# Optimization experiments

Measured on AMD Instinct MI355X. Metric: run time of the kernel, lower is better.

Reference implementation:

```python
import jax, jax.numpy as jnp
import numpy as np

N_HEADS, D_MODEL, D_K, D_V = 16, 1024, 64, 64
B, S = 2, 2048

def setup_inputs() -> dict:
    key = jax.random.key(0)
    k = jax.random.split(key, 7)
    s = 1.0 / np.sqrt(D_MODEL)
    return {
        "input_Q": jax.random.normal(k[0], (B, S, D_MODEL), jnp.float32),
        "input_K": jax.random.normal(k[1], (B, S, D_MODEL), jnp.float32),
        "input_V": jax.random.normal(k[2], (B, S, D_MODEL), jnp.float32),
        "W_Q": jax.random.normal(k[3], (D_MODEL, N_HEADS * D_K), jnp.float32) * s,
        "W_K": jax.random.normal(k[4], (D_MODEL, N_HEADS * D_K), jnp.float32) * s,
        "W_V": jax.random.normal(k[5], (D_MODEL, N_HEADS * D_V), jnp.float32) * s,
        "W_O": jax.random.normal(k[6], (N_HEADS * D_V, D_MODEL), jnp.float32) * s,
    }

def reference(input_Q, input_K, input_V, W_Q, W_K, W_V, W_O):
    b = input_Q.shape[0]
    # project and split heads: [b, h, s, d]
    Q = (input_Q @ W_Q).reshape(b, -1, N_HEADS, D_K).transpose(0, 2, 1, 3)
    K = (input_K @ W_K).reshape(b, -1, N_HEADS, D_K).transpose(0, 2, 1, 3)
    V = (input_V @ W_V).reshape(b, -1, N_HEADS, D_V).transpose(0, 2, 1, 3)
    scores = jnp.einsum("bhqd,bhkd->bhqk", Q, K) / np.sqrt(D_K)
    attn = jax.nn.softmax(scores, axis=-1)
    context = jnp.einsum("bhqk,bhkd->bhqd", attn, V)
    context = context.transpose(0, 2, 1, 3).reshape(b, -1, N_HEADS * D_V)
    out = context @ W_O + input_Q  # residual
    # LayerNorm instantiated fresh in torch forward -> gamma=1, beta=0
    mu = jnp.mean(out, axis=-1, keepdims=True)
    var = jnp.var(out, axis=-1, keepdims=True)
    return (out - mu) / jnp.sqrt(var + 1e-5)
```

## Files before the change

kernel.cpp:

```cpp
#include <hip/hip_runtime.h>
#include <hip/hip_bf16.h>
#include <cstdint>
#include <cstddef>

#define DEVFN __device__ __forceinline__

typedef __attribute__((ext_vector_type(8))) short short8;
typedef __attribute__((ext_vector_type(4))) float f32x4;
typedef __attribute__((ext_vector_type(16))) float f32x16;
typedef __attribute__((ext_vector_type(4))) unsigned short us4;

static constexpr int S_LEN = 2048;
static constexpr int DM    = 1024;
static constexpr int H     = 16;
static constexpr int DK    = 64;
static constexpr int BATCH = 2;
static constexpr int MROWS = BATCH * S_LEN;

DEVFN unsigned short f2bf(float f) {
  union { float f; unsigned int u; } x; x.f = f;
  unsigned int r = x.u + 0x7fffu + ((x.u >> 16) & 1u);
  return (unsigned short)(r >> 16);
}

DEVFN float fast_exp2(float x) { return __builtin_amdgcn_exp2f(x); }

DEVFN f32x4 mfma16(short8 a, short8 b, f32x4 c) {
  return __builtin_amdgcn_mfma_f32_16x16x32_bf16(a, b, c, 0, 0, 0);
}

DEVFN f32x16 mfma32(short8 a, short8 b, f32x16 c) {
  return __builtin_amdgcn_mfma_f32_32x32x16_bf16(a, b, c, 0, 0, 0);
}

DEVFN unsigned int cvtpk(float lo, float hi) {
  unsigned int r;
  asm("v_cvt_pk_bf16_f32 %0, %1, %2" : "=v"(r) : "v"(lo), "v"(hi));
  return r;
}

DEVFN void gload_lds16(const void* g, void* l) {
  __builtin_amdgcn_global_load_lds(
      (const __attribute__((address_space(1))) void*)g,
      (__attribute__((address_space(3))) void*)l, 16, 0, 0);
}

__global__ __launch_bounds__(256) void wt_transpose(
    const float* __restrict__ Wq, const float* __restrict__ Wk,
    const float* __restrict__ Wv, const float* __restrict__ Wo,
    unsigned short* __restrict__ Tq, unsigned short* __restrict__ Tk,
    unsigned short* __restrict__ Tv, unsigned short* __restrict__ To)
{
  const float* W = blockIdx.z == 0 ? Wq : blockIdx.z == 1 ? Wk : blockIdx.z == 2 ? Wv : Wo;
  unsigned short* T = blockIdx.z == 0 ? Tq : blockIdx.z == 1 ? Tk : blockIdx.z == 2 ? Tv : To;
  __shared__ float tile[32][33];
  int n0 = blockIdx.x * 32, k0 = blockIdx.y * 32;
  int tx = threadIdx.x & 31, ty = threadIdx.x >> 5;
#pragma unroll
  for (int i = 0; i < 4; ++i)
    tile[ty + 8 * i][tx] = W[(size_t)(k0 + ty + 8 * i) * DM + n0 + tx];
  __syncthreads();
#pragma unroll
  for (int i = 0; i < 4; ++i) {
    int n = ty + 8 * i;
    T[(size_t)(n0 + n) * DM + k0 + tx] = f2bf(tile[tx][n]);
  }
}

__global__ __launch_bounds__(256) void xcvt3(
    const float* __restrict__ X0, const float* __restrict__ X1,
    const float* __restrict__ X2, unsigned short* __restrict__ Y)
{
  const float* X = blockIdx.y == 0 ? X0 : blockIdx.y == 1 ? X1 : X2;
  unsigned short* Yz = Y + (size_t)blockIdx.y * MROWS * DM;
  const size_t i = ((size_t)blockIdx.x * 256 + threadIdx.x) * 8;
  float4 v0 = *(const float4*)(X + i);
  float4 v1 = *(const float4*)(X + i + 4);
  union { us4 u[2]; short8 s; } r;
  r.u[0].x = f2bf(v0.x); r.u[0].y = f2bf(v0.y); r.u[0].z = f2bf(v0.z); r.u[0].w = f2bf(v0.w);
  r.u[1].x = f2bf(v1.x); r.u[1].y = f2bf(v1.y); r.u[1].z = f2bf(v1.z); r.u[1].w = f2bf(v1.w);
  *(short8*)(Yz + i) = r.s;
}

__global__ __launch_bounds__(256, 3) void gemm_qkv(
    const unsigned short* __restrict__ Xb,
    const unsigned short* __restrict__ Tq, const unsigned short* __restrict__ Tk,
    const unsigned short* __restrict__ Tv,
    unsigned short* __restrict__ Qb, unsigned short* __restrict__ Kb,
    unsigned short* __restrict__ Vt)
{
  __shared__ __align__(16) unsigned short As[2][128 * 32];
  __shared__ __align__(16) unsigned short Bs[2][128 * 32];

  const int z = blockIdx.z;
  const unsigned short* A = Xb + (size_t)z * MROWS * DM;
  const unsigned short* T = z == 0 ? Tq : z == 1 ? Tk : Tv;

  const int tid = threadIdx.x;
  const int lane = tid & 63, w = tid >> 6;
  const int wm = w >> 1, wn = w & 1;
  const int lr = lane & 15, lg = lane >> 4;
  const int m0 = blockIdx.x * 128, n0 = blockIdx.y * 128;

  const int srw = lane >> 2, sch = lane & 3;

  auto stage = [&](int buf, int k0) {
#pragma unroll
    for (int i = 0; i < 2; ++i) {
      const int rr = (w * 2 + i) * 16 + srw;
      const int sc = (sch ^ ((rr >> 1) & 3)) * 8;
      gload_lds16(A + (size_t)(m0 + rr) * DM + k0 + sc, &As[buf][(w * 2 + i) * 512]);
      gload_lds16(T + (size_t)(n0 + rr) * DM + k0 + sc, &Bs[buf][(w * 2 + i) * 512]);
    }
  };

  f32x4 acc[4][4];
#pragma unroll
  for (int m = 0; m < 4; ++m)
#pragma unroll
    for (int n = 0; n < 4; ++n) acc[m][n] = (f32x4){0.f, 0.f, 0.f, 0.f};

  stage(0, 0);

  int buf = 0;
  for (int kt = 0; kt < DM / 32; ++kt) {
    if (kt + 1 < DM / 32) {
      stage(buf ^ 1, (kt + 1) * 32);
      asm volatile("s_waitcnt vmcnt(4)");
    } else {
      asm volatile("s_waitcnt vmcnt(0)");
    }
    __builtin_amdgcn_s_barrier();

    short8 af[4], bfr[4];
#pragma unroll
    for (int m = 0; m < 4; ++m) {
      const int row = wm * 64 + m * 16 + lr;
      const int ch = lg ^ ((row >> 1) & 3);
      af[m] = *(const short8*)&As[buf][row * 32 + ch * 8];
    }
#pragma unroll
    for (int n = 0; n < 4; ++n) {
      const int row = wn * 64 + n * 16 + lr;
      const int ch = lg ^ ((row >> 1) & 3);
      bfr[n] = *(const short8*)&Bs[buf][row * 32 + ch * 8];
    }
#pragma unroll
    for (int m = 0; m < 4; ++m)
#pragma unroll
      for (int n = 0; n < 4; ++n) acc[m][n] = mfma16(af[m], bfr[n], acc[m][n]);

    __builtin_amdgcn_s_barrier();
    buf ^= 1;
  }

  if (z < 2) {
    const float scale = (z == 0) ? 0.125f * 1.44269504088896f : 1.0f;
    unsigned short* out = z == 0 ? Qb : Kb;
#pragma unroll
    for (int m = 0; m < 4; ++m)
#pragma unroll
      for (int n = 0; n < 4; ++n) {
        int col = n0 + wn * 64 + n * 16 + lr;
        int h = col >> 6, d = col & 63;
#pragma unroll
        for (int r = 0; r < 4; ++r) {
          int row = m0 + wm * 64 + m * 16 + lg * 4 + r;
          int b = row >> 11, s = row & (S_LEN - 1);
          out[((size_t)(b * H + h) * S_LEN + s) * DK + d] = f2bf(acc[m][n][r] * scale);
        }
      }
  } else {
#pragma unroll
    for (int m = 0; m < 4; ++m)
#pragma unroll
      for (int n = 0; n < 4; ++n) {
        int col = n0 + wn * 64 + n * 16 + lr;
        int h = col >> 6, d = col & 63;
        int row = m0 + wm * 64 + m * 16 + lg * 4;
        int b = row >> 11, s = row & (S_LEN - 1);
        us4 u;
#pragma unroll
        for (int r = 0; r < 4; ++r) u[r] = f2bf(acc[m][n][r]);
        *(us4*)(Vt + ((size_t)(b * H + h) * DK + d) * S_LEN + s) = u;
      }
  }
}

__global__ __launch_bounds__(256, 2) void attn(
    const unsigned short* __restrict__ Qg, const unsigned short* __restrict__ Kg,
    const unsigned short* __restrict__ Vg, unsigned short* __restrict__ ctx)
{
  constexpr int KBLK = 64;
  constexpr int NT = S_LEN / KBLK;
  __shared__ __align__(16) unsigned short Ks[4][KBLK][DK];
  __shared__ __align__(16) unsigned short Vs[4][DK][KBLK];

  const int tid = threadIdx.x, lane = tid & 63, w = tid >> 6;
  const int l31 = lane & 31, hi = lane >> 5;

  const int orig = blockIdx.x;
  const int id = (orig & 7) * 64 + (orig >> 3);
  const int bh = id >> 4, qb = id & 15;
  const int b = bh >> 4, h = bh & 15;
  const int q = qb * 128 + w * 32 + l31;

  const unsigned short* Qbh = Qg + (size_t)bh * S_LEN * DK;
  const unsigned short* Kbh = Kg + (size_t)bh * S_LEN * DK;
  const unsigned short* Vbh = Vg + (size_t)bh * DK * S_LEN;

  const int srow = lane >> 3;
  const int sslot = ((lane & 7) ^ srow) * 8;

  auto stage = [&](int buf, int t) {
    const int kbase = t * KBLK;
#pragma unroll
    for (int c = 0; c < 2; ++c) {
      const int rbase = w * 8 + c * 32;
      gload_lds16(Kbh + (size_t)(kbase + rbase + srow) * DK + sslot, &Ks[buf][rbase][0]);
      gload_lds16(Vbh + (size_t)(rbase + srow) * S_LEN + kbase + sslot, &Vs[buf][rbase][0]);
    }
  };

  short8 qf[4];
#pragma unroll
  for (int kk = 0; kk < 4; ++kk)
    qf[kk] = *(const short8*)(Qbh + (size_t)q * DK + kk * 16 + hi * 8);

  f32x16 o0, o1;
#pragma unroll
  for (int i = 0; i < 16; ++i) { o0[i] = 0.f; o1[i] = 0.f; }
  float lrun = 0.f;

  const int swz = (l31 & 7) << 4;

  auto tile = [&](int buf) {
    const char* Kb = (const char*)&Ks[buf][0][0];
    const char* Vb = (const char*)&Vs[buf][0][0];

    f32x16 s0, s1;
#pragma unroll
    for (int i = 0; i < 16; ++i) { s0[i] = 0.f; s1[i] = 0.f; }
    __builtin_amdgcn_s_setprio(1);
#pragma unroll
    for (int kk = 0; kk < 4; ++kk) {
      const int cb = (kk * 32 + hi * 16) ^ swz;
      short8 ka0 = *(const short8*)(Kb + l31 * 128 + cb);
      short8 ka1 = *(const short8*)(Kb + (32 + l31) * 128 + cb);
      s0 = mfma32(ka0, qf[kk], s0);
      s1 = mfma32(ka1, qf[kk], s1);
    }
    __builtin_amdgcn_s_setprio(0);

#pragma unroll
    for (int i = 0; i < 16; ++i) {
      s0[i] = fast_exp2(s0[i]);
      s1[i] = fast_exp2(s1[i]);
    }

    float d0[16];
#pragma unroll
    for (int i = 0; i < 16; ++i) d0[i] = s0[i] + s1[i];
#pragma unroll
    for (int st = 8; st >= 1; st >>= 1)
#pragma unroll
      for (int i = 0; i < st; ++i) d0[i] = d0[i] + d0[i + st];
    lrun += d0[0] + __shfl_xor(d0[0], 32, 64);

    short8 pf[4];
#pragma unroll
    for (int sl = 0; sl < 4; ++sl) {
      const f32x16& sv = (sl & 2) ? s1 : s0;
      const int base = (sl & 1) * 8;
      const unsigned int a01 = cvtpk(sv[base + 0], sv[base + 1]);
      const unsigned int a23 = cvtpk(sv[base + 2], sv[base + 3]);
      const unsigned int b01 = cvtpk(sv[base + 4], sv[base + 5]);
      const unsigned int b23 = cvtpk(sv[base + 6], sv[base + 7]);
      const unsigned int x0 = __shfl_xor(hi ? a01 : b01, 32, 64);
      const unsigned int x1 = __shfl_xor(hi ? a23 : b23, 32, 64);
      union { unsigned int u[4]; short8 v; } pu;
      pu.u[0] = hi ? x0 : a01;
      pu.u[1] = hi ? x1 : a23;
      pu.u[2] = hi ? b01 : x0;
      pu.u[3] = hi ? b23 : x1;
      pf[sl] = pu.v;
    }

    __builtin_amdgcn_s_setprio(1);
#pragma unroll
    for (int sl = 0; sl < 4; ++sl) {
      const int cb = (sl * 32 + hi * 16) ^ swz;
      short8 va0 = *(const short8*)(Vb + l31 * 128 + cb);
      short8 va1 = *(const short8*)(Vb + (32 + l31) * 128 + cb);
      o0 = mfma32(va0, pf[sl], o0);
      o1 = mfma32(va1, pf[sl], o1);
    }
    __builtin_amdgcn_s_setprio(0);
  };

  stage(0, 0);
  stage(1, 1);

  for (int t = 0; t < NT; t += 2) {
    const bool more = (t + 2) < NT;
    if (more) {
      stage((t + 2) & 3, t + 2);
      stage((t + 3) & 3, t + 3);
      asm volatile("s_waitcnt vmcnt(8)");
    } else {
      asm volatile("s_waitcnt vmcnt(0)");
    }
    __builtin_amdgcn_s_barrier();
    tile(t & 3);
    tile((t + 1) & 3);
    __builtin_amdgcn_s_barrier();
  }

  const float rinv = 1.0f / lrun;
  unsigned short* crow = ctx + ((size_t)(b * S_LEN + q)) * DM + h * DK;
#pragma unroll
  for (int n = 0; n < 2; ++n) {
#pragma unroll
    for (int r = 0; r < 16; r += 2) {
      const float v0 = (n ? o1[r] : o0[r]) * rinv;
      const float v1 = (n ? o1[r + 1] : o0[r + 1]) * rinv;
      const int d = (r & 3) + 8 * (r >> 2) + 4 * hi + 32 * n;
      *(unsigned int*)(crow + d) = cvtpk(v0, v1);
    }
  }
}

__global__ __launch_bounds__(256, 3) void gemm_out(
    const unsigned short* __restrict__ C, const unsigned short* __restrict__ To,
    const float* __restrict__ resid, float* __restrict__ y)
{
  __shared__ __align__(16) unsigned short As[2][128 * 32];
  __shared__ __align__(16) unsigned short Bs[2][64 * 32];

  const int tid = threadIdx.x;
  const int lane = tid & 63, w = tid >> 6;
  const int wm = w >> 1, wn = w & 1;
  const int lr = lane & 15, lg = lane >> 4;
  const int m0 = blockIdx.x * 128, n0 = blockIdx.y * 64;

  const int brr = lane >> 2, bsc = lane & 3;

  auto stage = [&](int buf, int k0) {
#pragma unroll
    for (int i = 0; i < 2; ++i) {
      const int rr = (w * 2 + i) * 16 + brr;
      const int sc = (bsc ^ ((rr >> 1) & 3)) * 8;
      gload_lds16(C + (size_t)(m0 + rr) * DM + k0 + sc, &As[buf][(w * 2 + i) * 512]);
    }
    const int rr = w * 16 + brr;
    const int sc = (bsc ^ ((rr >> 1) & 3)) * 8;
    gload_lds16(To + (size_t)(n0 + rr) * DM + k0 + sc, &Bs[buf][w * 512]);
  };

  f32x4 acc[4][2];
#pragma unroll
  for (int m = 0; m < 4; ++m)
#pragma unroll
    for (int n = 0; n < 2; ++n) acc[m][n] = (f32x4){0.f, 0.f, 0.f, 0.f};

  stage(0, 0);

  int buf = 0;
  for (int kt = 0; kt < DM / 32; ++kt) {
    if (kt + 1 < DM / 32) {
      stage(buf ^ 1, (kt + 1) * 32);
      asm volatile("s_waitcnt vmcnt(3)");
    } else {
      asm volatile("s_waitcnt vmcnt(0)");
    }
    __builtin_amdgcn_s_barrier();

    short8 af[4], bfr[2];
#pragma unroll
    for (int m = 0; m < 4; ++m) {
      const int row = wm * 64 + m * 16 + lr;
      const int ch = lg ^ ((row >> 1) & 3);
      af[m] = *(const short8*)&As[buf][row * 32 + ch * 8];
    }
#pragma unroll
    for (int n = 0; n < 2; ++n) {
      const int row = wn * 32 + n * 16 + lr;
      const int ch = lg ^ ((row >> 1) & 3);
      bfr[n] = *(const short8*)&Bs[buf][row * 32 + ch * 8];
    }
#pragma unroll
    for (int m = 0; m < 4; ++m)
#pragma unroll
      for (int n = 0; n < 2; ++n) acc[m][n] = mfma16(af[m], bfr[n], acc[m][n]);

    __builtin_amdgcn_s_barrier();
    buf ^= 1;
  }

#pragma unroll
  for (int m = 0; m < 4; ++m)
#pragma unroll
    for (int n = 0; n < 2; ++n) {
      int col = n0 + wn * 32 + n * 16 + lr;
#pragma unroll
      for (int r = 0; r < 4; ++r) {
        int row = m0 + wm * 64 + m * 16 + lg * 4 + r;
        size_t idx = (size_t)row * DM + col;
        y[idx] = acc[m][n][r] + resid[idx];
      }
    }
}

__global__ __launch_bounds__(256) void lnorm(const float* __restrict__ y, float* __restrict__ out)
{
  const int row = blockIdx.x;
  const int tid = threadIdx.x;
  const float4 v = ((const float4*)(y + (size_t)row * DM))[tid];
  float s = v.x + v.y + v.z + v.w;
  float sq = v.x * v.x + v.y * v.y + v.z * v.z + v.w * v.w;
  s += __shfl_xor(s, 1, 64);  sq += __shfl_xor(sq, 1, 64);
  s += __shfl_xor(s, 2, 64);  sq += __shfl_xor(sq, 2, 64);
  s += __shfl_xor(s, 4, 64);  sq += __shfl_xor(sq, 4, 64);
  s += __shfl_xor(s, 8, 64);  sq += __shfl_xor(sq, 8, 64);
  s += __shfl_xor(s, 16, 64); sq += __shfl_xor(sq, 16, 64);
  s += __shfl_xor(s, 32, 64); sq += __shfl_xor(sq, 32, 64);
  __shared__ float ps[4], pq[4];
  int w = tid >> 6, lane = tid & 63;
  if (lane == 0) { ps[w] = s; pq[w] = sq; }
  __syncthreads();
  s = ps[0] + ps[1] + ps[2] + ps[3];
  sq = pq[0] + pq[1] + pq[2] + pq[3];
  float mean = s * (1.0f / DM);
  float var = sq * (1.0f / DM) - mean * mean;
  float rstd = rsqrtf(var + 1e-5f);
  float4 ov;
  ov.x = (v.x - mean) * rstd;
  ov.y = (v.y - mean) * rstd;
  ov.z = (v.z - mean) * rstd;
  ov.w = (v.w - mean) * rstd;
  ((float4*)(out + (size_t)row * DM))[tid] = ov;
}

extern "C" void kernel_launch(void* const* d_in, const int* in_sizes, int n_in,
                              void* d_out, int out_size, void* d_ws, size_t ws_size,
                              hipStream_t stream) {
  const float* Xq = (const float*)d_in[0];
  const float* Xk = (const float*)d_in[1];
  const float* Xv = (const float*)d_in[2];
  const float* Wq = (const float*)d_in[3];
  const float* Wk = (const float*)d_in[4];
  const float* Wv = (const float*)d_in[5];
  const float* Wo = (const float*)d_in[6];
  float* out = (float*)d_out;
  char* ws = (char*)d_ws;

  const size_t WT_BYTES  = (size_t)DM * DM * 2;
  const size_t XB_BYTES  = (size_t)3 * MROWS * DM * 2;
  const size_t QKV_BYTES = (size_t)BATCH * H * S_LEN * DK * 2;

  size_t off = 0;
  auto take = [&](size_t bytes) { size_t o = off; off += (bytes + 255) & ~(size_t)255; return o; };
  unsigned short* Tq  = (unsigned short*)(ws + take(WT_BYTES));
  unsigned short* Tk  = (unsigned short*)(ws + take(WT_BYTES));
  unsigned short* Tv  = (unsigned short*)(ws + take(WT_BYTES));
  unsigned short* To  = (unsigned short*)(ws + take(WT_BYTES));
  size_t xb_off = take(XB_BYTES);
  unsigned short* Xb  = (unsigned short*)(ws + xb_off);
  unsigned short* Qb  = (unsigned short*)(ws + take(QKV_BYTES));
  unsigned short* Kb  = (unsigned short*)(ws + take(QKV_BYTES));
  unsigned short* Vt  = (unsigned short*)(ws + take(QKV_BYTES));
  unsigned short* Ctx = Xb;
  float* y = (float*)(ws + xb_off + (size_t)MROWS * DM * 2);

  if (ws_size < off) return;

  wt_transpose<<<dim3(32, 32, 4), 256, 0, stream>>>(Wq, Wk, Wv, Wo, Tq, Tk, Tv, To);
  xcvt3<<<dim3(2048, 3), 256, 0, stream>>>(Xq, Xk, Xv, Xb);
  gemm_qkv<<<dim3(32, 8, 3), 256, 0, stream>>>(Xb, Tq, Tk, Tv, Qb, Kb, Vt);
  attn<<<dim3(512), 256, 0, stream>>>(Qb, Kb, Vt, Ctx);
  gemm_out<<<dim3(32, 16), 256, 0, stream>>>(Ctx, To, Xq, y);
  lnorm<<<MROWS, 256, 0, stream>>>(y, out);
}
```

Before: 125.0 us.

## Split attention KV range across two wave groups and merge partial outputs

The attention kernel now launches 512 threads per block, split into two groups of four waves. Each group handles half of the key/value sequence with its own double-buffered LDS region, and the partial outputs and row sums are combined through shared memory at the end. The aim is more waves in flight per query tile, giving better latency hiding and CU occupancy with only 512 blocks. The cost is an extra LDS reduction, a shallower prefetch depth (2 buffers instead of 4), and 64KB of LDS per block, which may limit how many blocks fit on a CU. It relies on a fixed softmax max (no running max), so partial sums can be added directly.

```diff
diff --git a/kernel.cpp b/kernel.cpp
--- a/kernel.cpp
+++ b/kernel.cpp
@@ -187,23 +187,23 @@
   }
 }
 
-__global__ __launch_bounds__(256, 2) void attn(
+__global__ __launch_bounds__(512, 4) void attn(
     const unsigned short* __restrict__ Qg, const unsigned short* __restrict__ Kg,
     const unsigned short* __restrict__ Vg, unsigned short* __restrict__ ctx)
 {
   constexpr int KBLK = 64;
-  constexpr int NT = S_LEN / KBLK;
-  __shared__ __align__(16) unsigned short Ks[4][KBLK][DK];
-  __shared__ __align__(16) unsigned short Vs[4][DK][KBLK];
+  __shared__ __align__(16) unsigned char smem[65536];
 
   const int tid = threadIdx.x, lane = tid & 63, w = tid >> 6;
+  const int wg = w >> 2, w4 = w & 3;
   const int l31 = lane & 31, hi = lane >> 5;
 
   const int orig = blockIdx.x;
   const int id = (orig & 7) * 64 + (orig >> 3);
   const int bh = id >> 4, qb = id & 15;
   const int b = bh >> 4, h = bh & 15;
-  const int q = qb * 128 + w * 32 + l31;
+  const int q = qb * 128 + w4 * 32 + l31;
+  const int t0 = wg * 16;
 
   const unsigned short* Qbh = Qg + (size_t)bh * S_LEN * DK;
   const unsigned short* Kbh = Kg + (size_t)bh * S_LEN * DK;
@@ -212,13 +212,18 @@
   const int srow = lane >> 3;
   const int sslot = ((lane & 7) ^ srow) * 8;
 
+  auto Kbuf = [&](int buf) { return (unsigned short*)(smem + (size_t)(wg * 2 + buf) * 16384); };
+  auto Vbuf = [&](int buf) { return (unsigned short*)(smem + (size_t)(wg * 2 + buf) * 16384 + 8192); };
+
   auto stage = [&](int buf, int t) {
     const int kbase = t * KBLK;
+    unsigned short* kb = Kbuf(buf);
+    unsigned short* vb = Vbuf(buf);
 #pragma unroll
     for (int c = 0; c < 2; ++c) {
-      const int rbase = w * 8 + c * 32;
-      gload_lds16(Kbh + (size_t)(kbase + rbase + srow) * DK + sslot, &Ks[buf][rbase][0]);
-      gload_lds16(Vbh + (size_t)(rbase + srow) * S_LEN + kbase + sslot, &Vs[buf][rbase][0]);
+      const int rbase = w4 * 8 + c * 32;
+      gload_lds16(Kbh + (size_t)(kbase + rbase + srow) * DK + sslot, kb + rbase * DK);
+      gload_lds16(Vbh + (size_t)(rbase + srow) * S_LEN + kbase + sslot, vb + rbase * DK);
     }
   };
 
@@ -235,8 +240,8 @@
   const int swz = (l31 & 7) << 4;
 
   auto tile = [&](int buf) {
-    const char* Kb = (const char*)&Ks[buf][0][0];
-    const char* Vb = (const char*)&Vs[buf][0][0];
+    const char* Kb = (const char*)Kbuf(buf);
+    const char* Vb = (const char*)Vbuf(buf);
 
     f32x16 s0, s1;
 #pragma unroll
@@ -298,34 +303,48 @@
     __builtin_amdgcn_s_setprio(0);
   };
 
-  stage(0, 0);
-  stage(1, 1);
-
-  for (int t = 0; t < NT; t += 2) {
-    const bool more = (t + 2) < NT;
-    if (more) {
-      stage((t + 2) & 3, t + 2);
-      stage((t + 3) & 3, t + 3);
-      asm volatile("s_waitcnt vmcnt(8)");
+  stage(0, t0);
+
+  int buf = 0;
+  for (int tt = 0; tt < 16; ++tt) {
+    if (tt + 1 < 16) {
+      stage(buf ^ 1, t0 + tt + 1);
+      asm volatile("s_waitcnt vmcnt(4)");
     } else {
       asm volatile("s_waitcnt vmcnt(0)");
     }
     __builtin_amdgcn_s_barrier();
-    tile(t & 3);
-    tile((t + 1) & 3);
+    tile(buf);
     __builtin_amdgcn_s_barrier();
-  }
-
-  const float rinv = 1.0f / lrun;
-  unsigned short* crow = ctx + ((size_t)(b * S_LEN + q)) * DM + h * DK;
-#pragma unroll
-  for (int n = 0; n < 2; ++n) {
-#pragma unroll
-    for (int r = 0; r < 16; r += 2) {
-      const float v0 = (n ? o1[r] : o0[r]) * rinv;
-      const float v1 = (n ? o1[r + 1] : o0[r + 1]) * rinv;
-      const int d = (r & 3) + 8 * (r >> 2) + 4 * hi + 32 * n;
-      *(unsigned int*)(crow + d) = cvtpk(v0, v1);
+    buf ^= 1;
+  }
+
+  __syncthreads();
+  float* cmb = (float*)smem;
+  if (wg == 1) {
+    float* dst = cmb + ((size_t)(w4 * 64 + lane)) * 33;
+#pragma unroll
+    for (int i = 0; i < 16; ++i) { dst[i] = o0[i]; dst[16 + i] = o1[i]; }
+    dst[32] = lrun;
+  }
+  __syncthreads();
+  if (wg == 0) {
+    const float* src = cmb + ((size_t)(w4 * 64 + lane)) * 33;
+#pragma unroll
+    for (int i = 0; i < 16; ++i) { o0[i] += src[i]; o1[i] += src[16 + i]; }
+    lrun += src[32];
+
+    const float rinv = 1.0f / lrun;
+    unsigned short* crow = ctx + ((size_t)(b * S_LEN + q)) * DM + h * DK;
+#pragma unroll
+    for (int n = 0; n < 2; ++n) {
+#pragma unroll
+      for (int r = 0; r < 16; r += 2) {
+        const float v0 = (n ? o1[r] : o0[r]) * rinv;
+        const float v1 = (n ? o1[r + 1] : o0[r + 1]) * rinv;
+        const int d = (r & 3) + 8 * (r >> 2) + 4 * hi + 32 * n;
+        *(unsigned int*)(crow + d) = cvtpk(v0, v1);
+      }
     }
   }
 }
@@ -477,7 +496,7 @@
   wt_transpose<<<dim3(32, 32, 4), 256, 0, stream>>>(Wq, Wk, Wv, Wo, Tq, Tk, Tv, To);
   xcvt3<<<dim3(2048, 3), 256, 0, stream>>>(Xq, Xk, Xv, Xb);
   gemm_qkv<<<dim3(32, 8, 3), 256, 0, stream>>>(Xb, Tq, Tk, Tv, Qb, Kb, Vt);
-  attn<<<dim3(512), 256, 0, stream>>>(Qb, Kb, Vt, Ctx);
+  attn<<<dim3(512), 512, 0, stream>>>(Qb, Kb, Vt, Ctx);
   gemm_out<<<dim3(32, 16), 256, 0, stream>>>(Ctx, To, Xq, y);
   lnorm<<<MROWS, 256, 0, stream>>>(y, out);
 }
```

New measurement: 124.5 us. No clear change (-0.4%).
